# Performance work log

Hardware: AMD Instinct MI355X
Metric: run time of the kernel (lower is better)

## Reference

```python
import jax, jax.numpy as jnp
import numpy as np

N_NODES = 100000


def _gcn_conv(x, src, dst, w, W, b, n):
    # x: [N, Fin]; src/dst: [E'] (self-loops already appended); w: [E']
    h = x @ W                                   # [N, Fout] linear first (Fout <= Fin)
    deg = jax.ops.segment_sum(w, dst, num_segments=n)          # weighted in-degree
    dinv = jnp.where(deg > 0, jax.lax.rsqrt(jnp.maximum(deg, 1e-12)), 0.0)
    norm = dinv[src] * w * dinv[dst]            # [E'] symmetric normalization
    msg = norm[:, None] * h[src]                # [E', Fout] gather + scale
    out = jax.ops.segment_sum(msg, dst, num_segments=n)        # scatter-add
    return out + b


def setup_inputs() -> dict:
    key = jax.random.key(0)
    k1, k2, k3, k4, k5 = jax.random.split(key, 5)
    N, E, Fin, Fh, Fo = N_NODES, 3200000, 256, 128, 64
    x = jax.random.normal(k1, (N, Fin), dtype=jnp.float32)
    edge_index = jax.random.randint(k2, (2, E), 0, N, dtype=jnp.int64)
    edge_weight = jax.random.uniform(k3, (E,), dtype=jnp.float32)
    W1 = jax.random.normal(k4, (Fin, Fh), dtype=jnp.float32) * (1.0 / np.sqrt(Fin))
    b1 = jnp.zeros((Fh,), dtype=jnp.float32)
    W2 = jax.random.normal(k5, (Fh, Fo), dtype=jnp.float32) * (1.0 / np.sqrt(Fh))
    b2 = jnp.zeros((Fo,), dtype=jnp.float32)
    return {"x": x, "edge_index": edge_index, "edge_weight": edge_weight,
            "W1": W1, "b1": b1, "W2": W2, "b2": b2}


def reference(x, edge_index, edge_weight, W1, b1, W2, b2):
    n = x.shape[0]
    loop = jnp.arange(n, dtype=edge_index.dtype)
    src = jnp.concatenate([edge_index[0], loop])
    dst = jnp.concatenate([edge_index[1], loop])
    w = jnp.concatenate([edge_weight, jnp.ones((n,), dtype=edge_weight.dtype)])
    h = _gcn_conv(x, src, dst, w, W1, b1, n)
    h = jax.nn.relu(h)
    out = _gcn_conv(h, src, dst, w, W2, b2, n)
    return out
```

## Files before the change

### kernel.cpp

```cpp
#include <hip/hip_runtime.h>
#include <hip/hip_bf16.h>
#include <hip/hip_fp16.h>


#define FIN 256
#define FH  128
#define FO  64

#define EBLK 8192
#define WFX  33554432.0f
#define WFXI (1.0f / 33554432.0f)

typedef short s16x8 __attribute__((ext_vector_type(8)));
typedef float f32x4 __attribute__((ext_vector_type(4)));
typedef float f32x2 __attribute__((ext_vector_type(2)));

__device__ __forceinline__ unsigned int f2h(float f) {
  union { _Float16 h; unsigned short s; } c; c.h = (_Float16)f;
  return (unsigned int)c.s;
}
__device__ __forceinline__ unsigned int f2bf(float f) {
  union { float f; unsigned int i; } c; c.f = f;
  unsigned int i = c.i;
  return (i + 0x7FFFu + ((i >> 16) & 1u)) >> 16;
}
__device__ __forceinline__ void cvt8(const uint4& v, float* f) {
  const __half2* hp = (const __half2*)&v;
  #pragma unroll
  for (int j = 0; j < 4; ++j) {
    float2 t = __half22float2(hp[j]);
    f[2 * j] = t.x; f[2 * j + 1] = t.y;
  }
}
__device__ __forceinline__ void cvt8q(const uint2& v, float* f) {
  f32x2 t0 = __builtin_amdgcn_cvt_pk_f32_fp8((int)v.x, false);
  f32x2 t1 = __builtin_amdgcn_cvt_pk_f32_fp8((int)v.x, true);
  f32x2 t2 = __builtin_amdgcn_cvt_pk_f32_fp8((int)v.y, false);
  f32x2 t3 = __builtin_amdgcn_cvt_pk_f32_fp8((int)v.y, true);
  f[0] = t0[0]; f[1] = t0[1]; f[2] = t1[0]; f[3] = t1[1];
  f[4] = t2[0]; f[5] = t2[1]; f[6] = t3[0]; f[7] = t3[1];
}

__global__ __launch_bounds__(256) void prep_w_kernel(
    const float* __restrict__ W1, const float* __restrict__ W2,
    unsigned short* __restrict__ WT1, unsigned short* __restrict__ WT2) {
  int i = blockIdx.x * 256 + threadIdx.x;
  if (i < FIN * FH) {
    int k = i >> 7, j = i & 127;
    WT1[j * FIN + k] = (unsigned short)f2bf(W1[i]);
  } else {
    int i2 = i - FIN * FH;
    if (i2 < FH * FO) {
      int k = i2 >> 6, j = i2 & 63;
      WT2[j * FH + k] = (unsigned short)f2bf(W2[i2]);
    }
  }
}

__global__ __launch_bounds__(256) void a1hist_gemm1_kernel(
    const int* __restrict__ dst, int* __restrict__ gtable, int E,
    int NBA, int NB,
    const float* __restrict__ X, const unsigned short* __restrict__ WT1,
    unsigned char* __restrict__ H1q, int N, int NBG) {
  __shared__ __align__(16) short XS[64 * 40];
  __shared__ __align__(16) short WTS[128 * 40];
  __shared__ unsigned int bh[392];
  int bid = blockIdx.x;
  int tid = threadIdx.x;
  if (bid < NBA) {
    for (int k = tid; k < NB; k += 256) bh[k] = 0u;
    __syncthreads();
    int e0 = bid * EBLK;
    #pragma unroll 4
    for (int it = 0; it < EBLK / 256; ++it) {
      int e = e0 + it * 256 + tid;
      if (e < E) atomicAdd(&bh[dst[e] >> 8], 1u);
    }
    __syncthreads();
    for (int k = tid; k < NB; k += 256)
      gtable[k * NBA + bid] = (int)bh[k];
    return;
  }
  int g = bid - NBA;
  if (g >= NBG) return;
  int row0 = g * 64;
  int wave = tid >> 6, lane = tid & 63;
  int lr = lane & 15, lq = lane >> 4;
  f32x4 acc[8];
  #pragma unroll
  for (int c = 0; c < 8; ++c) acc[c] = (f32x4)(0.f);

  for (int k0 = 0; k0 < FIN; k0 += 32) {
    {
      int row = tid >> 2, koff = (tid & 3) * 8;
      int gr = row0 + row;
      float4 va = make_float4(0.f, 0.f, 0.f, 0.f), vb = va;
      if (gr < N) {
        va = *(const float4*)(X + (size_t)gr * FIN + k0 + koff);
        vb = *(const float4*)(X + (size_t)gr * FIN + k0 + koff + 4);
      }
      s16x8 hv;
      hv[0] = (short)f2bf(va.x); hv[1] = (short)f2bf(va.y);
      hv[2] = (short)f2bf(va.z); hv[3] = (short)f2bf(va.w);
      hv[4] = (short)f2bf(vb.x); hv[5] = (short)f2bf(vb.y);
      hv[6] = (short)f2bf(vb.z); hv[7] = (short)f2bf(vb.w);
      *(s16x8*)(&XS[row * 40 + koff]) = hv;
    }
    {
      int j = tid >> 1, o = (tid & 1) * 16;
      uint4 v0 = *(const uint4*)(WT1 + (size_t)j * FIN + k0 + o);
      uint4 v1 = *(const uint4*)(WT1 + (size_t)j * FIN + k0 + o + 8);
      *(uint4*)(&WTS[j * 40 + o]) = v0;
      *(uint4*)(&WTS[j * 40 + o + 8]) = v1;
    }
    __syncthreads();
    s16x8 af = *(const s16x8*)(&XS[(wave * 16 + lr) * 40 + lq * 8]);
    #pragma unroll
    for (int c = 0; c < 8; ++c) {
      s16x8 bf = *(const s16x8*)(&WTS[(c * 16 + lr) * 40 + lq * 8]);
      acc[c] = __builtin_amdgcn_mfma_f32_16x16x32_bf16(af, bf, acc[c], 0, 0, 0);
    }
    __syncthreads();
  }
  int orow = row0 + wave * 16 + lq * 4;
  #pragma unroll
  for (int c = 0; c < 8; ++c) {
    #pragma unroll
    for (int r = 0; r < 4; ++r) {
      int gr = orow + r;
      if (gr < N) {
        int pk = __builtin_amdgcn_cvt_pk_fp8_f32(acc[c][r], acc[c][r], 0, false);
        H1q[(size_t)gr * FH + c * 16 + lr] = (unsigned char)(pk & 0xff);
      }
    }
  }
}

__global__ __launch_bounds__(256) void scan1i_kernel(
    int* __restrict__ arr, int* __restrict__ bsum, int L) {
  __shared__ int tot[256];
  int t = threadIdx.x;
  int base = blockIdx.x * 1024 + t * 4;
  int v0 = (base + 0 < L) ? arr[base + 0] : 0;
  int v1 = (base + 1 < L) ? arr[base + 1] : 0;
  int v2 = (base + 2 < L) ? arr[base + 2] : 0;
  int v3 = (base + 3 < L) ? arr[base + 3] : 0;
  int s = v0 + v1 + v2 + v3;
  tot[t] = s;
  __syncthreads();
  for (int off = 1; off < 256; off <<= 1) {
    int y = (t >= off) ? tot[t - off] : 0;
    __syncthreads();
    tot[t] += y;
    __syncthreads();
  }
  int p = tot[t] - s;
  if (t == 255) bsum[blockIdx.x] = tot[255];
  if (base + 0 < L) arr[base + 0] = p; p += v0;
  if (base + 1 < L) arr[base + 1] = p; p += v1;
  if (base + 2 < L) arr[base + 2] = p; p += v2;
  if (base + 3 < L) arr[base + 3] = p;
}

__global__ __launch_bounds__(256) void scan2_kernel(
    int* __restrict__ bsum, int nb) {
  __shared__ int buf[256];
  int t = threadIdx.x;
  int v = (t < nb) ? bsum[t] : 0;
  buf[t] = v;
  __syncthreads();
  for (int off = 1; off < 256; off <<= 1) {
    int y = (t >= off) ? buf[t - off] : 0;
    __syncthreads();
    buf[t] += y;
    __syncthreads();
  }
  if (t < nb) bsum[t] = buf[t] - v;
}

__global__ __launch_bounds__(256) void scan3_kernel(
    int* __restrict__ arr, const int* __restrict__ bsum, int L) {
  int i = blockIdx.x * 256 + threadIdx.x;
  if (i < L) arr[i] += bsum[i >> 10];
}

__global__ __launch_bounds__(1024) void a3_bucketize_kernel(
    const int* __restrict__ src, const int* __restrict__ dst,
    const float* __restrict__ w, const int* __restrict__ gtable,
    unsigned long long* __restrict__ bdw, int E, int NBA) {
  __shared__ unsigned int bh[392];
  int bid = blockIdx.x;
  int tid = threadIdx.x;
  for (int k = tid; k < 392; k += 1024) bh[k] = 0u;
  __syncthreads();
  int e0 = bid * EBLK;
  #pragma unroll 2
  for (int it = 0; it < EBLK / 1024; ++it) {
    int e = e0 + it * 1024 + tid;
    if (e < E) {
      int d = dst[e];
      int k = d >> 8;
      unsigned int l = (unsigned int)(d & 255);
      unsigned int r = atomicAdd(&bh[k], 1u);
      int pos = gtable[k * NBA + bid] + (int)r;
      unsigned int lo = (unsigned int)src[e] | (l << 20);
      unsigned long long v = ((unsigned long long)__float_as_uint(w[e]) << 32)
                           | (unsigned long long)lo;
      bdw[pos] = v;
    }
  }
}

__global__ __launch_bounds__(1024) void b1_degree_kernel(
    const unsigned long long* __restrict__ bdw,
    const int* __restrict__ gtable, int* __restrict__ rowptr,
    float* __restrict__ dinv, int E, int NBA, int NB, int N) {
  __shared__ unsigned int lcnt[256];
  __shared__ unsigned int lwfx[256];
  __shared__ int sc[256];
  int k = blockIdx.x;
  int t = threadIdx.x;
  if (t < 256) { lcnt[t] = 0u; lwfx[t] = 0u; }
  __syncthreads();
  int base = gtable[k * NBA];
  int end  = (k + 1 < NB) ? gtable[(k + 1) * NBA] : E;
  for (int i = base + t; i < end; i += 1024) {
    unsigned long long v = bdw[i];
    unsigned int lo = (unsigned int)v;
    unsigned int l = (lo >> 20) & 0xFFu;
    float wv = __uint_as_float((unsigned int)(v >> 32));
    atomicAdd(&lcnt[l], 1u);
    atomicAdd(&lwfx[l], (unsigned int)(wv * WFX));
  }
  __syncthreads();
  int c = 0;
  if (t < 256) { c = (int)lcnt[t]; sc[t] = c; }
  __syncthreads();
  for (int off = 1; off < 256; off <<= 1) {
    int y = (t >= off && t < 256) ? sc[t - off] : 0;
    __syncthreads();
    if (t < 256) sc[t] += y;
    __syncthreads();
  }
  if (t < 256) {
    int excl = sc[t] - c;
    int node = (k << 8) + t;
    if (node < N) {
      rowptr[node] = base + excl;
      float deg = (float)lwfx[t] * WFXI;
      dinv[node] = rsqrtf(1.0f + deg);
    }
  }
  if (k == 0 && t == 0) rowptr[N] = E;
}

__global__ __launch_bounds__(1024) void b2_scatter_kernel(
    const unsigned long long* __restrict__ bdw,
    const int* __restrict__ gtable, const int* __restrict__ rowptr,
    const float* __restrict__ dinv, int2* __restrict__ edges,
    int E, int NBA, int NB) {
  __shared__ unsigned int rcnt[256];
  int k = blockIdx.x;
  int t = threadIdx.x;
  if (t < 256) rcnt[t] = 0u;
  __syncthreads();
  int base = gtable[k * NBA];
  int end  = (k + 1 < NB) ? gtable[(k + 1) * NBA] : E;
  for (int i = base + t; i < end; i += 1024) {
    unsigned long long v = bdw[i];
    unsigned int lo = (unsigned int)v;
    int s = (int)(lo & 0xFFFFFu);
    unsigned int l = (lo >> 20) & 0xFFu;
    float wv = __uint_as_float((unsigned int)(v >> 32));
    unsigned int r = atomicAdd(&rcnt[l], 1u);
    int d = (k << 8) + (int)l;
    int pos = rowptr[d] + (int)r;
    float nm = dinv[s] * wv * dinv[d];
    edges[pos] = make_int2(s, __float_as_int(nm));
  }
}

__global__ __launch_bounds__(256) void gemm2_kernel(
    const unsigned short* __restrict__ A1b, const unsigned short* __restrict__ WT2,
    unsigned short* __restrict__ H2h, int N) {
  __shared__ __align__(16) short XS[64 * 40];
  __shared__ __align__(16) short WTS[64 * 40];
  int tid = threadIdx.x;
  int row0 = blockIdx.x * 64;
  int wave = tid >> 6, lane = tid & 63;
  int lr = lane & 15, lq = lane >> 4;
  f32x4 acc[4];
  #pragma unroll
  for (int c = 0; c < 4; ++c) acc[c] = (f32x4)(0.f);

  for (int k0 = 0; k0 < FH; k0 += 32) {
    {
      int row = tid >> 2, o = (tid & 3) * 8;
      int gr = row0 + row;
      uint4 v = make_uint4(0u, 0u, 0u, 0u);
      if (gr < N) v = *(const uint4*)(A1b + (size_t)gr * FH + k0 + o);
      *(uint4*)(&XS[row * 40 + o]) = v;
    }
    {
      int j = tid >> 2, o = (tid & 3) * 8;
      uint4 v = *(const uint4*)(WT2 + (size_t)j * FH + k0 + o);
      *(uint4*)(&WTS[j * 40 + o]) = v;
    }
    __syncthreads();
    s16x8 af = *(const s16x8*)(&XS[(wave * 16 + lr) * 40 + lq * 8]);
    #pragma unroll
    for (int c = 0; c < 4; ++c) {
      s16x8 bf = *(const s16x8*)(&WTS[(c * 16 + lr) * 40 + lq * 8]);
      acc[c] = __builtin_amdgcn_mfma_f32_16x16x32_bf16(af, bf, acc[c], 0, 0, 0);
    }
    __syncthreads();
  }
  int orow = row0 + wave * 16 + lq * 4;
  #pragma unroll
  for (int c = 0; c < 4; ++c) {
    #pragma unroll
    for (int r = 0; r < 4; ++r) {
      int gr = orow + r;
      if (gr < N)
        H2h[(size_t)gr * FO + c * 16 + lr] = (unsigned short)f2h(acc[c][r]);
    }
  }
}

__global__ __launch_bounds__(256) void agg1_kernel(
    const unsigned char* __restrict__ H1q, const int2* __restrict__ edges,
    const int* __restrict__ rowptr, const float* __restrict__ dinv,
    const float* __restrict__ b1, unsigned short* __restrict__ A1b, int N) {
  int wid = (blockIdx.x * 256 + threadIdx.x) >> 6;
  int lane = threadIdx.x & 63;
  if (wid >= N) return;
  int p0 = rowptr[wid], p1 = rowptr[wid + 1];
  int grp = lane >> 4, li = lane & 15;
  const size_t rowoff = (size_t)li * 8;
  float a0[8], a1v[8], a2v[8];
  #pragma unroll
  for (int j = 0; j < 8; ++j) { a0[j] = 0.f; a1v[j] = 0.f; a2v[j] = 0.f; }

  int p = p0;
  for (; p + 12 <= p1; p += 12) {
    int2 e0 = edges[p + grp];
    int2 e1 = edges[p + 4 + grp];
    int2 e2 = edges[p + 8 + grp];
    uint2 h0 = *(const uint2*)(H1q + (size_t)e0.x * FH + rowoff);
    uint2 h1 = *(const uint2*)(H1q + (size_t)e1.x * FH + rowoff);
    uint2 h2 = *(const uint2*)(H1q + (size_t)e2.x * FH + rowoff);
    float n0 = __int_as_float(e0.y), n1 = __int_as_float(e1.y);
    float n2 = __int_as_float(e2.y);
    float f0[8], f1[8], f2[8];
    cvt8q(h0, f0); cvt8q(h1, f1); cvt8q(h2, f2);
    #pragma unroll
    for (int j = 0; j < 8; ++j) {
      a0[j] += n0 * f0[j];
      a1v[j] += n1 * f1[j];
      a2v[j] += n2 * f2[j];
    }
  }
  for (; p + 4 <= p1; p += 4) {
    int2 e0 = edges[p + grp];
    uint2 h0 = *(const uint2*)(H1q + (size_t)e0.x * FH + rowoff);
    float n0 = __int_as_float(e0.y);
    float f0[8];
    cvt8q(h0, f0);
    #pragma unroll
    for (int j = 0; j < 8; ++j) a0[j] += n0 * f0[j];
  }
  if (p < p1) {
    int q = p + grp;
    int qi = (q < p1) ? q : p;
    int2 e0 = edges[qi];
    float n0 = (q < p1) ? __int_as_float(e0.y) : 0.f;
    uint2 h0 = *(const uint2*)(H1q + (size_t)e0.x * FH + rowoff);
    float f0[8];
    cvt8q(h0, f0);
    #pragma unroll
    for (int j = 0; j < 8; ++j) a0[j] += n0 * f0[j];
  }
  float s[8];
  #pragma unroll
  for (int j = 0; j < 8; ++j) {
    s[j] = (a0[j] + a1v[j]) + a2v[j];
    s[j] += __shfl_xor(s[j], 16);
    s[j] += __shfl_xor(s[j], 32);
  }
  if (lane < 16) {
    float di = dinv[wid], sn = di * di;
    uint2 hs = *(const uint2*)(H1q + (size_t)wid * FH + rowoff);
    float fs[8];
    cvt8q(hs, fs);
    #pragma unroll
    for (int j = 0; j < 8; ++j) s[j] += sn * fs[j];
    float4 bv0 = *(const float4*)(b1 + li * 8);
    float4 bv1 = *(const float4*)(b1 + li * 8 + 4);
    s[0] = fmaxf(s[0] + bv0.x, 0.f); s[1] = fmaxf(s[1] + bv0.y, 0.f);
    s[2] = fmaxf(s[2] + bv0.z, 0.f); s[3] = fmaxf(s[3] + bv0.w, 0.f);
    s[4] = fmaxf(s[4] + bv1.x, 0.f); s[5] = fmaxf(s[5] + bv1.y, 0.f);
    s[6] = fmaxf(s[6] + bv1.z, 0.f); s[7] = fmaxf(s[7] + bv1.w, 0.f);
    uint4 pk;
    pk.x = f2bf(s[0]) | (f2bf(s[1]) << 16);
    pk.y = f2bf(s[2]) | (f2bf(s[3]) << 16);
    pk.z = f2bf(s[4]) | (f2bf(s[5]) << 16);
    pk.w = f2bf(s[6]) | (f2bf(s[7]) << 16);
    *(uint4*)(A1b + (size_t)wid * FH + li * 8) = pk;
  }
}

__global__ __launch_bounds__(256) void agg2_kernel(
    const unsigned short* __restrict__ H2h, const int2* __restrict__ edges,
    const int* __restrict__ rowptr, const float* __restrict__ dinv,
    const float* __restrict__ b2, float* __restrict__ OUT, int N) {
  int wid = (blockIdx.x * 256 + threadIdx.x) >> 6;
  int lane = threadIdx.x & 63;
  if (wid >= N) return;
  int p0 = rowptr[wid], p1 = rowptr[wid + 1];
  int grp = lane >> 3, li = lane & 7;
  const size_t rowoff = (size_t)li * 8;
  float a0[8], a1v[8];
  #pragma unroll
  for (int j = 0; j < 8; ++j) { a0[j] = 0.f; a1v[j] = 0.f; }

  int p = p0;
  for (; p + 16 <= p1; p += 16) {
    int2 e0 = edges[p + grp];
    int2 e1 = edges[p + 8 + grp];
    uint4 h0 = *(const uint4*)(H2h + (size_t)e0.x * FO + rowoff);
    uint4 h1 = *(const uint4*)(H2h + (size_t)e1.x * FO + rowoff);
    float n0 = __int_as_float(e0.y), n1 = __int_as_float(e1.y);
    float f0[8], f1[8];
    cvt8(h0, f0); cvt8(h1, f1);
    #pragma unroll
    for (int j = 0; j < 8; ++j) {
      a0[j] += n0 * f0[j];
      a1v[j] += n1 * f1[j];
    }
  }
  for (; p + 8 <= p1; p += 8) {
    int2 e0 = edges[p + grp];
    uint4 h0 = *(const uint4*)(H2h + (size_t)e0.x * FO + rowoff);
    float n0 = __int_as_float(e0.y);
    float f0[8];
    cvt8(h0, f0);
    #pragma unroll
    for (int j = 0; j < 8; ++j) a0[j] += n0 * f0[j];
  }
  if (p < p1) {
    int q = p + grp;
    int qi = (q < p1) ? q : p;
    int2 e0 = edges[qi];
    float n0 = (q < p1) ? __int_as_float(e0.y) : 0.f;
    uint4 h0 = *(const uint4*)(H2h + (size_t)e0.x * FO + rowoff);
    float f0[8];
    cvt8(h0, f0);
    #pragma unroll
    for (int j = 0; j < 8; ++j) a0[j] += n0 * f0[j];
  }
  float s[8];
  #pragma unroll
  for (int j = 0; j < 8; ++j) {
    s[j] = a0[j] + a1v[j];
    s[j] += __shfl_xor(s[j], 8);
    s[j] += __shfl_xor(s[j], 16);
    s[j] += __shfl_xor(s[j], 32);
  }
  if (lane < 8) {
    float di = dinv[wid], sn = di * di;
    uint4 hs = *(const uint4*)(H2h + (size_t)wid * FO + rowoff);
    float fs[8];
    cvt8(hs, fs);
    #pragma unroll
    for (int j = 0; j < 8; ++j) s[j] += sn * fs[j];
    float4 bv0 = *(const float4*)(b2 + li * 8);
    float4 bv1 = *(const float4*)(b2 + li * 8 + 4);
    float4 o0 = make_float4(s[0] + bv0.x, s[1] + bv0.y, s[2] + bv0.z, s[3] + bv0.w);
    float4 o1 = make_float4(s[4] + bv1.x, s[5] + bv1.y, s[6] + bv1.z, s[7] + bv1.w);
    *(float4*)(OUT + (size_t)wid * FO + li * 8) = o0;
    *(float4*)(OUT + (size_t)wid * FO + li * 8 + 4) = o1;
  }
}

extern "C" void kernel_launch(void* const* d_in, const int* in_sizes, int n_in,
                              void* d_out, int out_size, void* d_ws, size_t ws_size,
                              hipStream_t stream) {
  const float* x  = (const float*)d_in[0];
  const int*   ei = (const int*)d_in[1];
  const float* ew = (const float*)d_in[2];
  const float* W1 = (const float*)d_in[3];
  const float* b1 = (const float*)d_in[4];
  const float* W2 = (const float*)d_in[5];
  const float* b2 = (const float*)d_in[6];
  float* out = (float*)d_out;

  const int N = in_sizes[0] / FIN;
  const int E = in_sizes[2];
  const int* src = ei;
  const int* dst = ei + E;
  const int NBG = (N + 63) / 64;
  const int NBA = (E + EBLK - 1) / EBLK;
  const int NB  = (N + 255) / 256;
  const int L   = NB * NBA;
  const int nsb = (L + 1023) / 1024;

  char* ws = (char*)d_ws;
  size_t off = 0;
  unsigned char*  h1q = (unsigned char*)(ws + off);  off += (size_t)N * FH;
  unsigned short* h2h = (unsigned short*)(ws + off); off += (size_t)N * FO * 2;
  unsigned short* a1b = (unsigned short*)(ws + off); off += (size_t)N * FH * 2;
  int2*  edges  = (int2*) (ws + off); off += (size_t)E * 8;
  unsigned long long* bdw = (unsigned long long*)(ws + off); off += (size_t)E * 8;
  int*   gtable = (int*)  (ws + off); off += (((size_t)L * 4) + 15) & ~(size_t)15;
  int*   rowptr = (int*)  (ws + off); off += (((size_t)(N + 1) * 4) + 15) & ~(size_t)15;
  float* dinv   = (float*)(ws + off); off += (size_t)N * 4;
  int*   bsum   = (int*)  (ws + off); off += 1024;
  unsigned short* WT1 = (unsigned short*)(ws + off); off += (size_t)FH * FIN * 2;
  unsigned short* WT2 = (unsigned short*)(ws + off); off += (size_t)FO * FH * 2;

  prep_w_kernel<<<(FIN * FH + FH * FO + 255) / 256, 256, 0, stream>>>(W1, W2, WT1, WT2);
  a1hist_gemm1_kernel<<<NBA + NBG, 256, 0, stream>>>(dst, gtable, E, NBA, NB,
                                                     x, WT1, h1q, N, NBG);
  scan1i_kernel<<<nsb, 256, 0, stream>>>(gtable, bsum, L);
  scan2_kernel<<<1, 256, 0, stream>>>(bsum, nsb);
  scan3_kernel<<<(L + 255) / 256, 256, 0, stream>>>(gtable, bsum, L);
  a3_bucketize_kernel<<<NBA, 1024, 0, stream>>>(src, dst, ew, gtable, bdw, E, NBA);
  b1_degree_kernel<<<NB, 1024, 0, stream>>>(bdw, gtable, rowptr, dinv, E, NBA, NB, N);
  b2_scatter_kernel<<<NB, 1024, 0, stream>>>(bdw, gtable, rowptr, dinv, edges,
                                             E, NBA, NB);
  agg1_kernel<<<(N * 64 + 255) / 256, 256, 0, stream>>>(h1q, edges, rowptr,
                                                        dinv, b1, a1b, N);
  gemm2_kernel<<<(N + 63) / 64, 256, 0, stream>>>(a1b, WT2, h2h, N);
  agg2_kernel<<<(N * 64 + 255) / 256, 256, 0, stream>>>(h2h, edges, rowptr,
                                                        dinv, b2, out, N);
}
```

Measured before the change: 309.2 us.

## Fuse degree and scatter kernels, defer source normalization to aggregation

```diff
diff --git a/kernel.cpp b/kernel.cpp
--- a/kernel.cpp
+++ b/kernel.cpp
@@ -7,7 +7,7 @@
 #define FH  128
 #define FO  64
 
-#define EBLK 8192
+#define EBLK 2048
 #define WFX  33554432.0f
 #define WFXI (1.0f / 33554432.0f)
 
@@ -140,12 +140,14 @@
     int* __restrict__ arr, int* __restrict__ bsum, int L) {
   __shared__ int tot[256];
   int t = threadIdx.x;
-  int base = blockIdx.x * 1024 + t * 4;
-  int v0 = (base + 0 < L) ? arr[base + 0] : 0;
-  int v1 = (base + 1 < L) ? arr[base + 1] : 0;
-  int v2 = (base + 2 < L) ? arr[base + 2] : 0;
-  int v3 = (base + 3 < L) ? arr[base + 3] : 0;
-  int s = v0 + v1 + v2 + v3;
+  int base = blockIdx.x * 4096 + t * 16;
+  int v[16];
+  int s = 0;
+  #pragma unroll
+  for (int q = 0; q < 16; ++q) {
+    v[q] = (base + q < L) ? arr[base + q] : 0;
+    s += v[q];
+  }
   tot[t] = s;
   __syncthreads();
   for (int off = 1; off < 256; off <<= 1) {
@@ -156,10 +158,11 @@
   }
   int p = tot[t] - s;
   if (t == 255) bsum[blockIdx.x] = tot[255];
-  if (base + 0 < L) arr[base + 0] = p; p += v0;
-  if (base + 1 < L) arr[base + 1] = p; p += v1;
-  if (base + 2 < L) arr[base + 2] = p; p += v2;
-  if (base + 3 < L) arr[base + 3] = p;
+  #pragma unroll
+  for (int q = 0; q < 16; ++q) {
+    if (base + q < L) arr[base + q] = p;
+    p += v[q];
+  }
 }
 
 __global__ __launch_bounds__(256) void scan2_kernel(
@@ -181,7 +184,7 @@
 __global__ __launch_bounds__(256) void scan3_kernel(
     int* __restrict__ arr, const int* __restrict__ bsum, int L) {
   int i = blockIdx.x * 256 + threadIdx.x;
-  if (i < L) arr[i] += bsum[i >> 10];
+  if (i < L) arr[i] += bsum[i >> 12];
 }
 
 __global__ __launch_bounds__(1024) void a3_bucketize_kernel(
@@ -194,7 +197,7 @@
   for (int k = tid; k < 392; k += 1024) bh[k] = 0u;
   __syncthreads();
   int e0 = bid * EBLK;
-  #pragma unroll 2
+  #pragma unroll
   for (int it = 0; it < EBLK / 1024; ++it) {
     int e = e0 + it * 1024 + tid;
     if (e < E) {
@@ -211,13 +214,16 @@
   }
 }
 
-__global__ __launch_bounds__(1024) void b1_degree_kernel(
+__global__ __launch_bounds__(1024) void b12_kernel(
     const unsigned long long* __restrict__ bdw,
     const int* __restrict__ gtable, int* __restrict__ rowptr,
-    float* __restrict__ dinv, int E, int NBA, int NB, int N) {
+    float* __restrict__ dinv, int2* __restrict__ edges,
+    int E, int NBA, int NB, int N) {
   __shared__ unsigned int lcnt[256];
   __shared__ unsigned int lwfx[256];
   __shared__ int sc[256];
+  __shared__ int lrp[256];
+  __shared__ float ldv[256];
   int k = blockIdx.x;
   int t = threadIdx.x;
   if (t < 256) { lcnt[t] = 0u; lwfx[t] = 0u; }
@@ -244,39 +250,29 @@
   }
   if (t < 256) {
     int excl = sc[t] - c;
+    int rp = base + excl;
+    lrp[t] = rp;
+    float di = rsqrtf(1.0f + (float)lwfx[t] * WFXI);
+    ldv[t] = di;
     int node = (k << 8) + t;
     if (node < N) {
-      rowptr[node] = base + excl;
-      float deg = (float)lwfx[t] * WFXI;
-      dinv[node] = rsqrtf(1.0f + deg);
-    }
+      rowptr[node] = rp;
+      dinv[node] = di;
+    }
+    lcnt[t] = 0u;
   }
   if (k == 0 && t == 0) rowptr[N] = E;
-}
-
-__global__ __launch_bounds__(1024) void b2_scatter_kernel(
-    const unsigned long long* __restrict__ bdw,
-    const int* __restrict__ gtable, const int* __restrict__ rowptr,
-    const float* __restrict__ dinv, int2* __restrict__ edges,
-    int E, int NBA, int NB) {
-  __shared__ unsigned int rcnt[256];
-  int k = blockIdx.x;
-  int t = threadIdx.x;
-  if (t < 256) rcnt[t] = 0u;
-  __syncthreads();
-  int base = gtable[k * NBA];
-  int end  = (k + 1 < NB) ? gtable[(k + 1) * NBA] : E;
+  __syncthreads();
   for (int i = base + t; i < end; i += 1024) {
     unsigned long long v = bdw[i];
     unsigned int lo = (unsigned int)v;
     int s = (int)(lo & 0xFFFFFu);
     unsigned int l = (lo >> 20) & 0xFFu;
     float wv = __uint_as_float((unsigned int)(v >> 32));
-    unsigned int r = atomicAdd(&rcnt[l], 1u);
-    int d = (k << 8) + (int)l;
-    int pos = rowptr[d] + (int)r;
-    float nm = dinv[s] * wv * dinv[d];
-    edges[pos] = make_int2(s, __float_as_int(nm));
+    unsigned int r = atomicAdd(&lcnt[l], 1u);
+    int pos = lrp[l] + (int)r;
+    float wd = wv * ldv[l];
+    edges[pos] = make_int2(s, __float_as_int(wd));
   }
 }
 
@@ -349,8 +345,9 @@
     uint2 h0 = *(const uint2*)(H1q + (size_t)e0.x * FH + rowoff);
     uint2 h1 = *(const uint2*)(H1q + (size_t)e1.x * FH + rowoff);
     uint2 h2 = *(const uint2*)(H1q + (size_t)e2.x * FH + rowoff);
-    float n0 = __int_as_float(e0.y), n1 = __int_as_float(e1.y);
-    float n2 = __int_as_float(e2.y);
+    float n0 = __int_as_float(e0.y) * dinv[e0.x];
+    float n1 = __int_as_float(e1.y) * dinv[e1.x];
+    float n2 = __int_as_float(e2.y) * dinv[e2.x];
     float f0[8], f1[8], f2[8];
     cvt8q(h0, f0); cvt8q(h1, f1); cvt8q(h2, f2);
     #pragma unroll
@@ -363,7 +360,7 @@
   for (; p + 4 <= p1; p += 4) {
     int2 e0 = edges[p + grp];
     uint2 h0 = *(const uint2*)(H1q + (size_t)e0.x * FH + rowoff);
-    float n0 = __int_as_float(e0.y);
+    float n0 = __int_as_float(e0.y) * dinv[e0.x];
     float f0[8];
     cvt8q(h0, f0);
     #pragma unroll
@@ -373,7 +370,7 @@
     int q = p + grp;
     int qi = (q < p1) ? q : p;
     int2 e0 = edges[qi];
-    float n0 = (q < p1) ? __int_as_float(e0.y) : 0.f;
+    float n0 = (q < p1) ? __int_as_float(e0.y) * dinv[e0.x] : 0.f;
     uint2 h0 = *(const uint2*)(H1q + (size_t)e0.x * FH + rowoff);
     float f0[8];
     cvt8q(h0, f0);
@@ -429,7 +426,8 @@
     int2 e1 = edges[p + 8 + grp];
     uint4 h0 = *(const uint4*)(H2h + (size_t)e0.x * FO + rowoff);
     uint4 h1 = *(const uint4*)(H2h + (size_t)e1.x * FO + rowoff);
-    float n0 = __int_as_float(e0.y), n1 = __int_as_float(e1.y);
+    float n0 = __int_as_float(e0.y) * dinv[e0.x];
+    float n1 = __int_as_float(e1.y) * dinv[e1.x];
     float f0[8], f1[8];
     cvt8(h0, f0); cvt8(h1, f1);
     #pragma unroll
@@ -441,7 +439,7 @@
   for (; p + 8 <= p1; p += 8) {
     int2 e0 = edges[p + grp];
     uint4 h0 = *(const uint4*)(H2h + (size_t)e0.x * FO + rowoff);
-    float n0 = __int_as_float(e0.y);
+    float n0 = __int_as_float(e0.y) * dinv[e0.x];
     float f0[8];
     cvt8(h0, f0);
     #pragma unroll
@@ -451,7 +449,7 @@
     int q = p + grp;
     int qi = (q < p1) ? q : p;
     int2 e0 = edges[qi];
-    float n0 = (q < p1) ? __int_as_float(e0.y) : 0.f;
+    float n0 = (q < p1) ? __int_as_float(e0.y) * dinv[e0.x] : 0.f;
     uint4 h0 = *(const uint4*)(H2h + (size_t)e0.x * FO + rowoff);
     float f0[8];
     cvt8(h0, f0);
@@ -502,7 +500,7 @@
   const int NBA = (E + EBLK - 1) / EBLK;
   const int NB  = (N + 255) / 256;
   const int L   = NB * NBA;
-  const int nsb = (L + 1023) / 1024;
+  const int nsb = (L + 4095) / 4096;
 
   char* ws = (char*)d_ws;
   size_t off = 0;
@@ -525,9 +523,8 @@
   scan2_kernel<<<1, 256, 0, stream>>>(bsum, nsb);
   scan3_kernel<<<(L + 255) / 256, 256, 0, stream>>>(gtable, bsum, L);
   a3_bucketize_kernel<<<NBA, 1024, 0, stream>>>(src, dst, ew, gtable, bdw, E, NBA);
-  b1_degree_kernel<<<NB, 1024, 0, stream>>>(bdw, gtable, rowptr, dinv, E, NBA, NB, N);
-  b2_scatter_kernel<<<NB, 1024, 0, stream>>>(bdw, gtable, rowptr, dinv, edges,
-                                             E, NBA, NB);
+  b12_kernel<<<NB, 1024, 0, stream>>>(bdw, gtable, rowptr, dinv, edges,
+                                      E, NBA, NB, N);
   agg1_kernel<<<(N * 64 + 255) / 256, 256, 0, stream>>>(h1q, edges, rowptr,
                                                         dinv, b1, a1b, N);
   gemm2_kernel<<<(N + 63) / 64, 256, 0, stream>>>(a1b, WT2, h2h, N);
```

Result: no change. 308.5 us (-0.2%).
